# Performance work log

Measured on AMD Instinct MI355X. Metric: run time of the kernel, lower is better.

## Reference

```python
import jax, jax.numpy as jnp
import numpy as np

N_NODES = 50000
N_EDGES = 800000
IN_DIM = 128
HID = 64
N_GRAPHS = 256


def gcn_conv(x, W, b, src, dst, num_nodes):
    """PyG GCNConv: add self-loops, sym norm D^-1/2 (A+I) D^-1/2, linear, bias."""
    h = x @ W  # [N, out]
    loop = jnp.arange(num_nodes)
    s = jnp.concatenate([src, loop])
    d = jnp.concatenate([dst, loop])
    ones = jnp.ones(d.shape, h.dtype)
    deg = jax.ops.segment_sum(ones, d, num_segments=num_nodes)
    dinv = jnp.where(deg > 0, jax.lax.rsqrt(deg), 0.0)
    norm = dinv[s] * dinv[d]  # [E+N]
    msg = h[s] * norm[:, None]  # gather + scale (memory bound)
    out = jax.ops.segment_sum(msg, d, num_segments=num_nodes)  # scatter-add
    return out + b


def setup_inputs() -> dict:
    key = jax.random.key(0)
    ks = jax.random.split(key, 8)
    x = jax.random.normal(ks[0], (N_NODES, IN_DIM), dtype=jnp.float32)
    edge_index = jax.random.randint(ks[1], (2, N_EDGES), 0, N_NODES, dtype=jnp.int64)
    batch = jnp.sort(jax.random.randint(ks[2], (N_NODES,), 0, N_GRAPHS, dtype=jnp.int64))
    W1 = jax.random.normal(ks[3], (IN_DIM, HID), dtype=jnp.float32) / np.sqrt(IN_DIM)
    b1 = jnp.zeros((HID,), jnp.float32)
    W2 = jax.random.normal(ks[4], (HID, HID), dtype=jnp.float32) / np.sqrt(HID)
    b2 = jnp.zeros((HID,), jnp.float32)
    Wl = jax.random.normal(ks[5], (HID, 1), dtype=jnp.float32) / np.sqrt(HID)
    bl = jnp.zeros((1,), jnp.float32)
    return {"x": x, "W1": W1, "b1": b1, "W2": W2, "b2": b2,
            "Wl": Wl, "bl": bl, "edge_index": edge_index, "batch": batch}


def reference(x, W1, b1, W2, b2, Wl, bl, edge_index, batch):
    n = x.shape[0]
    src, dst = edge_index[0], edge_index[1]
    h = jax.nn.relu(gcn_conv(x, W1, b1, src, dst, n))
    # dropout is identity in eval mode
    h = jax.nn.relu(gcn_conv(h, W2, b2, src, dst, n))
    ones = jnp.ones((n,), h.dtype)
    counts = jax.ops.segment_sum(ones, batch, num_segments=N_GRAPHS)
    pooled = jax.ops.segment_sum(h, batch, num_segments=N_GRAPHS)
    pooled = pooled / jnp.maximum(counts, 1.0)[:, None]  # global_mean_pool
    return (pooled @ Wl + bl).reshape(-1)  # [N_GRAPHS]
```

## Files before the change

kernel.cpp:

```cpp
#include <hip/hip_runtime.h>
#include <math.h>

__global__ void zero32(int* __restrict__ p, int n) {
    int i = blockIdx.x * blockDim.x + threadIdx.x;
    if (i < n) p[i] = 0;
}

__global__ void hist_dst(const int* __restrict__ dst, int* __restrict__ cnt, int E) {
    int e = blockIdx.x * blockDim.x + threadIdx.x;
    if (e < E) atomicAdd(&cnt[dst[e]], 1);
}

__global__ __launch_bounds__(256) void scan1_dinv(const int* __restrict__ cnt,
                                                  int* __restrict__ excl,
                                                  int* __restrict__ sums,
                                                  float* __restrict__ dinv, int n) {
    int i = blockIdx.x * 256 + threadIdx.x;
    int v = (i < n) ? cnt[i] : 0;
    if (i < n) dinv[i] = rsqrtf((float)(v + 1));
    int lane = threadIdx.x & 63;
    int w = threadIdx.x >> 6;
    int s = v;
#pragma unroll
    for (int off = 1; off < 64; off <<= 1) {
        int t = __shfl_up(s, off, 64);
        if (lane >= off) s += t;
    }
    __shared__ int wsum[4];
    if (lane == 63) wsum[w] = s;
    __syncthreads();
    int woff = 0;
#pragma unroll
    for (int k = 0; k < 3; ++k) if (k < w) woff += wsum[k];
    int incl = s + woff;
    if (i < n) excl[i] = incl - v;
    if (threadIdx.x == 255) sums[blockIdx.x] = incl;
}

__global__ __launch_bounds__(256) void scan2(int* __restrict__ sums, int nb) {
    int t = threadIdx.x;
    int v = (t < nb) ? sums[t] : 0;
    int lane = t & 63;
    int w = t >> 6;
    int s = v;
#pragma unroll
    for (int off = 1; off < 64; off <<= 1) {
        int u = __shfl_up(s, off, 64);
        if (lane >= off) s += u;
    }
    __shared__ int wsum[4];
    if (lane == 63) wsum[w] = s;
    __syncthreads();
    int woff = 0;
#pragma unroll
    for (int k = 0; k < 3; ++k) if (k < w) woff += wsum[k];
    int incl = s + woff;
    if (t < nb) sums[t] = incl - v;
}

__global__ __launch_bounds__(256) void scan3(const int* __restrict__ excl,
                                             const int* __restrict__ sums,
                                             int* __restrict__ rowptr,
                                             int* __restrict__ cursor, int n, int E) {
    int i = blockIdx.x * 256 + threadIdx.x;
    if (i < n) {
        int r = excl[i] + sums[i >> 8];
        rowptr[i] = r;
        cursor[i] = r;
    }
    if (i == n) rowptr[n] = E;
}

__global__ void fill_col16(const int* __restrict__ src, const int* __restrict__ dst,
                           int* __restrict__ cursor, unsigned short* __restrict__ col,
                           int E, int n) {
    const int g    = blockIdx.x & 7;
    const int nblk = gridDim.x >> 3;
    const int bid  = blockIdx.x >> 3;
    const int lo = (int)(((long)g * n) >> 3);
    const int hi = (int)(((long)(g + 1) * n) >> 3);
    for (long e = (long)bid * blockDim.x + threadIdx.x; e < E;
         e += (long)nblk * blockDim.x) {
        int d = dst[e];
        if (d < lo || d >= hi) continue;
        int p = atomicAdd(&cursor[d], 1);
        col[p] = (unsigned short)src[e];
    }
}

#define RL(x, k) __int_as_float(__builtin_amdgcn_readlane(__float_as_int(x), (k)))

template <int K>
__global__ __launch_bounds__(256) void gemm_bcast_scaled(const float* __restrict__ X,
                                                         const float* __restrict__ W,
                                                         const float* __restrict__ dinv,
                                                         float* __restrict__ Y, int n) {
    const int lane = threadIdx.x & 63;
    const long wid = (((long)blockIdx.x * blockDim.x) + threadIdx.x) >> 6;
    const long nw  = ((long)gridDim.x * blockDim.x) >> 6;

    float wr[K];
#pragma unroll
    for (int k = 0; k < K; ++k) wr[k] = W[k * 64 + lane];
#pragma unroll
    for (int k = 0; k < K; ++k) asm volatile("" : "+v"(wr[k]));

    long r = wid;
    if (r >= n) return;
    float xa = X[r * K + lane];
    float xb = 0.f;
    if constexpr (K > 64) xb = X[r * K + 64 + lane];
    float dv = dinv[r];

    while (true) {
        long rn = r + nw;
        bool more = rn < n;
        long rc = more ? rn : r;
        float xan = X[rc * K + lane];
        float xbn = 0.f;
        if constexpr (K > 64) xbn = X[rc * K + 64 + lane];
        float dvn = dinv[rc];

        float a0 = 0.f, a1 = 0.f, a2 = 0.f, a3 = 0.f;
#pragma unroll
        for (int k = 0; k < 64; k += 4) {
            a0 = fmaf(RL(xa, k + 0), wr[k + 0], a0);
            a1 = fmaf(RL(xa, k + 1), wr[k + 1], a1);
            a2 = fmaf(RL(xa, k + 2), wr[k + 2], a2);
            a3 = fmaf(RL(xa, k + 3), wr[k + 3], a3);
        }
        if constexpr (K > 64) {
#pragma unroll
            for (int k = 0; k < 64; k += 4) {
                a0 = fmaf(RL(xb, k + 0), wr[64 + k + 0], a0);
                a1 = fmaf(RL(xb, k + 1), wr[64 + k + 1], a1);
                a2 = fmaf(RL(xb, k + 2), wr[64 + k + 2], a2);
                a3 = fmaf(RL(xb, k + 3), wr[64 + k + 3], a3);
            }
        }
        Y[r * 64 + lane] = dv * ((a0 + a1) + (a2 + a3));
        if (!more) break;
        r = rn;
        xa = xan;
        xb = xbn;
        dv = dvn;
    }
}

__device__ __forceinline__ void agg2(const float* __restrict__ Hp,
                                     const int* __restrict__ rowptr,
                                     const unsigned short* __restrict__ col,
                                     long vA, long vB, int j, bool hasB,
                                     float& sumA, float& sumB) {
    float a0 = Hp[vA * 64 + j], a1 = 0.f, a2 = 0.f, a3 = 0.f;
    float b0 = 0.f, b1 = 0.f, b2 = 0.f, b3 = 0.f;
    int pA = rowptr[vA], pA1 = rowptr[vA + 1];
    int pB = 0, pB1 = 0;
    if (hasB) { b0 = Hp[vB * 64 + j]; pB = rowptr[vB]; pB1 = rowptr[vB + 1]; }
    if ((pA & 1) && pA < pA1) { a1 += Hp[(long)col[pA] * 64 + j]; ++pA; }
    if ((pB & 1) && pB < pB1) { b1 += Hp[(long)col[pB] * 64 + j]; ++pB; }
    unsigned int cA01 = *(const unsigned int*)(col + pA);
    unsigned int cA23 = *(const unsigned int*)(col + pA + 2);
    unsigned int cB01 = *(const unsigned int*)(col + pB);
    unsigned int cB23 = *(const unsigned int*)(col + pB + 2);
    while (pA + 4 <= pA1 && pB + 4 <= pB1) {
        unsigned int nA01 = *(const unsigned int*)(col + pA + 4);
        unsigned int nA23 = *(const unsigned int*)(col + pA + 6);
        unsigned int nB01 = *(const unsigned int*)(col + pB + 4);
        unsigned int nB23 = *(const unsigned int*)(col + pB + 6);
        float hA0 = Hp[(long)(cA01 & 0xFFFFu) * 64 + j];
        float hA1 = Hp[(long)(cA01 >> 16) * 64 + j];
        float hA2 = Hp[(long)(cA23 & 0xFFFFu) * 64 + j];
        float hA3 = Hp[(long)(cA23 >> 16) * 64 + j];
        float hB0 = Hp[(long)(cB01 & 0xFFFFu) * 64 + j];
        float hB1 = Hp[(long)(cB01 >> 16) * 64 + j];
        float hB2 = Hp[(long)(cB23 & 0xFFFFu) * 64 + j];
        float hB3 = Hp[(long)(cB23 >> 16) * 64 + j];
        a0 += hA0; a1 += hA1; a2 += hA2; a3 += hA3;
        b0 += hB0; b1 += hB1; b2 += hB2; b3 += hB3;
        cA01 = nA01; cA23 = nA23; cB01 = nB01; cB23 = nB23;
        pA += 4; pB += 4;
    }
    for (; pA + 4 <= pA1; pA += 4) {
        float h0 = Hp[(long)(cA01 & 0xFFFFu) * 64 + j];
        float h1 = Hp[(long)(cA01 >> 16) * 64 + j];
        float h2 = Hp[(long)(cA23 & 0xFFFFu) * 64 + j];
        float h3 = Hp[(long)(cA23 >> 16) * 64 + j];
        a0 += h0; a1 += h1; a2 += h2; a3 += h3;
        cA01 = *(const unsigned int*)(col + pA + 4);
        cA23 = *(const unsigned int*)(col + pA + 6);
    }
    for (; pA < pA1; ++pA) a1 += Hp[(long)col[pA] * 64 + j];
    for (; pB + 4 <= pB1; pB += 4) {
        float h0 = Hp[(long)(cB01 & 0xFFFFu) * 64 + j];
        float h1 = Hp[(long)(cB01 >> 16) * 64 + j];
        float h2 = Hp[(long)(cB23 & 0xFFFFu) * 64 + j];
        float h3 = Hp[(long)(cB23 >> 16) * 64 + j];
        b0 += h0; b1 += h1; b2 += h2; b3 += h3;
        cB01 = *(const unsigned int*)(col + pB + 4);
        cB23 = *(const unsigned int*)(col + pB + 6);
    }
    for (; pB < pB1; ++pB) b1 += Hp[(long)col[pB] * 64 + j];
    sumA = (a0 + a1) + (a2 + a3);
    sumB = (b0 + b1) + (b2 + b3);
}

__global__ __launch_bounds__(256) void agg_gemm64(const float* __restrict__ Hp,
                                                  const int* __restrict__ rowptr,
                                                  const unsigned short* __restrict__ col,
                                                  const float* __restrict__ dinv,
                                                  const float* __restrict__ bias,
                                                  const float* __restrict__ W2,
                                                  float* __restrict__ out, int n) {
    const int j = threadIdx.x & 63;
    const long wid = (((long)blockIdx.x * blockDim.x) + threadIdx.x) >> 6;
    const long NW  = ((long)gridDim.x * blockDim.x) >> 6;
    float wr[64];
#pragma unroll
    for (int k = 0; k < 64; ++k) wr[k] = W2[k * 64 + j];
#pragma unroll
    for (int k = 0; k < 64; ++k) asm volatile("" : "+v"(wr[k]));
    const float bj = bias[j];
    for (long vA = wid; vA < n; vA += 2 * NW) {
        long vB = vA + NW;
        bool hasB = vB < n;
        float sA, sB;
        agg2(Hp, rowptr, col, vA, vB, j, hasB, sA, sB);
        float diA = dinv[vA];
        float diB = hasB ? dinv[vB] : 0.f;
        float gA = fmaxf(diA * sA + bj, 0.f);
        float gB = fmaxf(diB * sB + bj, 0.f);
        float a0 = 0.f, a1 = 0.f, a2 = 0.f, a3 = 0.f;
        float b0 = 0.f, b1 = 0.f, b2 = 0.f, b3 = 0.f;
#pragma unroll
        for (int k = 0; k < 64; k += 4) {
            float w0 = wr[k + 0], w1 = wr[k + 1], w2 = wr[k + 2], w3 = wr[k + 3];
            a0 = fmaf(RL(gA, k + 0), w0, a0);
            b0 = fmaf(RL(gB, k + 0), w0, b0);
            a1 = fmaf(RL(gA, k + 1), w1, a1);
            b1 = fmaf(RL(gB, k + 1), w1, b1);
            a2 = fmaf(RL(gA, k + 2), w2, a2);
            b2 = fmaf(RL(gB, k + 2), w2, b2);
            a3 = fmaf(RL(gA, k + 3), w3, a3);
            b3 = fmaf(RL(gB, k + 3), w3, b3);
        }
        out[vA * 64 + j] = diA * ((a0 + a1) + (a2 + a3));
        if (hasB) out[vB * 64 + j] = diB * ((b0 + b1) + (b2 + b3));
    }
}

__global__ __launch_bounds__(256) void agg_pool(const float* __restrict__ Hp,
                                                const int* __restrict__ rowptr,
                                                const unsigned short* __restrict__ col,
                                                const float* __restrict__ dinv,
                                                const float* __restrict__ bias,
                                                const float* __restrict__ Wl,
                                                const int* __restrict__ batch,
                                                float* __restrict__ part,
                                                float* __restrict__ partc, int n) {
    __shared__ float lp[256];
    __shared__ float lc[256];
    lp[threadIdx.x] = 0.f;
    lc[threadIdx.x] = 0.f;
    __syncthreads();
    const int j  = threadIdx.x & 63;
    const int wv = threadIdx.x >> 6;
    const float bj  = bias[j];
    const float wlj = Wl[j];
    const long wid = (long)blockIdx.x * 4 + wv;
    const long NW  = (long)gridDim.x * 4;
    for (long vA = wid; vA < n; vA += 2 * NW) {
        long vB = vA + NW;
        bool hasB = vB < n;
        float sA, sB;
        agg2(Hp, rowptr, col, vA, vB, j, hasB, sA, sB);
        float diA = dinv[vA];
        float diB = hasB ? dinv[vB] : 0.f;
        float valA = fmaxf(diA * sA + bj, 0.f) * wlj;
        float valB = fmaxf(diB * sB + bj, 0.f) * wlj;
#pragma unroll
        for (int off = 32; off > 0; off >>= 1) {
            valA += __shfl_down(valA, off, 64);
            valB += __shfl_down(valB, off, 64);
        }
        if (j == 0) {
            atomicAdd(&lp[batch[vA]], valA);
            atomicAdd(&lc[batch[vA]], 1.0f);
            if (hasB) {
                atomicAdd(&lp[batch[vB]], valB);
                atomicAdd(&lc[batch[vB]], 1.0f);
            }
        }
    }
    __syncthreads();
    long o = (long)blockIdx.x * 256 + threadIdx.x;
    part[o]  = lp[threadIdx.x];
    partc[o] = lc[threadIdx.x];
}

__global__ __launch_bounds__(256) void pool_final(const float* __restrict__ part,
                                                  const float* __restrict__ partc,
                                                  const float* __restrict__ bl,
                                                  float* __restrict__ out, int nblk) {
    int g = blockIdx.x;
    int t = threadIdx.x;
    float s = 0.f, c = 0.f;
    for (int b = t; b < nblk; b += 256) {
        s += part[(long)b * 256 + g];
        c += partc[(long)b * 256 + g];
    }
    __shared__ float sp[256];
    __shared__ float sc[256];
    sp[t] = s;
    sc[t] = c;
    __syncthreads();
    for (int off = 128; off > 0; off >>= 1) {
        if (t < off) { sp[t] += sp[t + off]; sc[t] += sc[t + off]; }
        __syncthreads();
    }
    if (t == 0) out[g] = sp[0] / fmaxf(sc[0], 1.0f) + bl[0];
}

extern "C" void kernel_launch(void* const* d_in, const int* in_sizes, int n_in,
                              void* d_out, int out_size, void* d_ws, size_t ws_size,
                              hipStream_t stream) {
    const float* x  = (const float*)d_in[0];
    const float* W1 = (const float*)d_in[1];
    const float* b1 = (const float*)d_in[2];
    const float* W2 = (const float*)d_in[3];
    const float* b2 = (const float*)d_in[4];
    const float* Wl = (const float*)d_in[5];
    const float* bl = (const float*)d_in[6];
    const int* edge_index = (const int*)d_in[7];
    const int* batch      = (const int*)d_in[8];

    const int n = in_sizes[0] / 128;
    const int E = in_sizes[7] / 2;
    const int G = out_size;
    const int* src = edge_index;
    const int* dst = edge_index + E;

    char* ws = (char*)d_ws;
    size_t off = 0;
    auto alloc = [&](size_t bytes) { void* p = ws + off; off = (off + bytes + 255) & ~(size_t)255; return p; };
    int*            cntv   = (int*)           alloc((size_t)n * 4);
    float*          dinv   = (float*)         alloc((size_t)n * 4);
    int*            rowptr = (int*)           alloc((size_t)(n + 1) * 4);
    int*            cursor = (int*)           alloc((size_t)n * 4);
    int*            excl   = (int*)           alloc((size_t)n * 4);
    int*            sums   = (int*)           alloc((size_t)256 * 4);
    unsigned short* col    = (unsigned short*)alloc((size_t)E * 2 + 64);
    float*          bufA   = (float*)         alloc((size_t)n * 64 * 4);
    float*          bufB   = (float*)         alloc((size_t)n * 64 * 4);
    const int PBLK = 2048;
    float*          part   = (float*)         alloc((size_t)PBLK * 256 * 4);
    float*          partc  = (float*)         alloc((size_t)PBLK * 256 * 4);

    const int T = 256;
    const int nchunks = (n + 255) / 256;
    zero32<<<(n + T - 1) / T, T, 0, stream>>>(cntv, n);
    hist_dst<<<(E + T - 1) / T, T, 0, stream>>>(dst, cntv, E);
    scan1_dinv<<<nchunks, T, 0, stream>>>(cntv, excl, sums, dinv, n);
    scan2<<<1, T, 0, stream>>>(sums, nchunks);
    scan3<<<(n + 1 + T - 1) / T, T, 0, stream>>>(excl, sums, rowptr, cursor, n, E);
    fill_col16<<<1024, T, 0, stream>>>(src, dst, cursor, col, E, n);

    gemm_bcast_scaled<128><<<768, T, 0, stream>>>(x, W1, dinv, bufA, n);
    agg_gemm64<<<2048, T, 0, stream>>>(bufA, rowptr, col, dinv, b1, W2, bufB, n);
    agg_pool<<<PBLK, T, 0, stream>>>(bufB, rowptr, col, dinv, b2, Wl, batch, part, partc, n);
    pool_final<<<G, T, 0, stream>>>(part, partc, bl, (float*)d_out, PBLK);
}
```

Before: 203.4 us.

## Record edge rank in histogram pass and add 2-deep prefetch in GEMM

```diff
diff --git a/kernel.cpp b/kernel.cpp
--- a/kernel.cpp
+++ b/kernel.cpp
@@ -6,9 +6,10 @@
     if (i < n) p[i] = 0;
 }
 
-__global__ void hist_dst(const int* __restrict__ dst, int* __restrict__ cnt, int E) {
+__global__ void hist_rank(const int* __restrict__ dst, int* __restrict__ cnt,
+                          unsigned short* __restrict__ rank, int E) {
     int e = blockIdx.x * blockDim.x + threadIdx.x;
-    if (e < E) atomicAdd(&cnt[dst[e]], 1);
+    if (e < E) rank[e] = (unsigned short)atomicAdd(&cnt[dst[e]], 1);
 }
 
 __global__ __launch_bounds__(256) void scan1_dinv(const int* __restrict__ cnt,
@@ -60,20 +61,16 @@
 
 __global__ __launch_bounds__(256) void scan3(const int* __restrict__ excl,
                                              const int* __restrict__ sums,
-                                             int* __restrict__ rowptr,
-                                             int* __restrict__ cursor, int n, int E) {
+                                             int* __restrict__ rowptr, int n, int E) {
     int i = blockIdx.x * 256 + threadIdx.x;
-    if (i < n) {
-        int r = excl[i] + sums[i >> 8];
-        rowptr[i] = r;
-        cursor[i] = r;
-    }
+    if (i < n) rowptr[i] = excl[i] + sums[i >> 8];
     if (i == n) rowptr[n] = E;
 }
 
-__global__ void fill_col16(const int* __restrict__ src, const int* __restrict__ dst,
-                           int* __restrict__ cursor, unsigned short* __restrict__ col,
-                           int E, int n) {
+__global__ void fill_place(const int* __restrict__ src, const int* __restrict__ dst,
+                           const unsigned short* __restrict__ rank,
+                           const int* __restrict__ rowptr,
+                           unsigned short* __restrict__ col, int E, int n) {
     const int g    = blockIdx.x & 7;
     const int nblk = gridDim.x >> 3;
     const int bid  = blockIdx.x >> 3;
@@ -83,8 +80,7 @@
          e += (long)nblk * blockDim.x) {
         int d = dst[e];
         if (d < lo || d >= hi) continue;
-        int p = atomicAdd(&cursor[d], 1);
-        col[p] = (unsigned short)src[e];
+        col[rowptr[d] + rank[e]] = (unsigned short)src[e];
     }
 }
 
@@ -105,45 +101,51 @@
 #pragma unroll
     for (int k = 0; k < K; ++k) asm volatile("" : "+v"(wr[k]));
 
-    long r = wid;
-    if (r >= n) return;
-    float xa = X[r * K + lane];
-    float xb = 0.f;
-    if constexpr (K > 64) xb = X[r * K + 64 + lane];
-    float dv = dinv[r];
+    long r0 = wid;
+    if (r0 >= n) return;
+    float xa0 = X[r0 * K + lane];
+    float xb0 = 0.f;
+    if constexpr (K > 64) xb0 = X[r0 * K + 64 + lane];
+    float dv0 = dinv[r0];
+
+    long r1 = r0 + nw;
+    bool h1 = r1 < n;
+    long rc1 = h1 ? r1 : r0;
+    float xa1 = X[rc1 * K + lane];
+    float xb1 = 0.f;
+    if constexpr (K > 64) xb1 = X[rc1 * K + 64 + lane];
+    float dv1 = dinv[rc1];
 
     while (true) {
-        long rn = r + nw;
-        bool more = rn < n;
-        long rc = more ? rn : r;
-        float xan = X[rc * K + lane];
-        float xbn = 0.f;
-        if constexpr (K > 64) xbn = X[rc * K + 64 + lane];
-        float dvn = dinv[rc];
+        long r2 = r1 + nw;
+        bool h2 = h1 && (r2 < n);
+        long rc2 = h2 ? r2 : r0;
+        float xa2 = X[rc2 * K + lane];
+        float xb2 = 0.f;
+        if constexpr (K > 64) xb2 = X[rc2 * K + 64 + lane];
+        float dv2 = dinv[rc2];
 
         float a0 = 0.f, a1 = 0.f, a2 = 0.f, a3 = 0.f;
 #pragma unroll
         for (int k = 0; k < 64; k += 4) {
-            a0 = fmaf(RL(xa, k + 0), wr[k + 0], a0);
-            a1 = fmaf(RL(xa, k + 1), wr[k + 1], a1);
-            a2 = fmaf(RL(xa, k + 2), wr[k + 2], a2);
-            a3 = fmaf(RL(xa, k + 3), wr[k + 3], a3);
+            a0 = fmaf(RL(xa0, k + 0), wr[k + 0], a0);
+            a1 = fmaf(RL(xa0, k + 1), wr[k + 1], a1);
+            a2 = fmaf(RL(xa0, k + 2), wr[k + 2], a2);
+            a3 = fmaf(RL(xa0, k + 3), wr[k + 3], a3);
         }
         if constexpr (K > 64) {
 #pragma unroll
             for (int k = 0; k < 64; k += 4) {
-                a0 = fmaf(RL(xb, k + 0), wr[64 + k + 0], a0);
-                a1 = fmaf(RL(xb, k + 1), wr[64 + k + 1], a1);
-                a2 = fmaf(RL(xb, k + 2), wr[64 + k + 2], a2);
-                a3 = fmaf(RL(xb, k + 3), wr[64 + k + 3], a3);
+                a0 = fmaf(RL(xb0, k + 0), wr[64 + k + 0], a0);
+                a1 = fmaf(RL(xb0, k + 1), wr[64 + k + 1], a1);
+                a2 = fmaf(RL(xb0, k + 2), wr[64 + k + 2], a2);
+                a3 = fmaf(RL(xb0, k + 3), wr[64 + k + 3], a3);
             }
         }
-        Y[r * 64 + lane] = dv * ((a0 + a1) + (a2 + a3));
-        if (!more) break;
-        r = rn;
-        xa = xan;
-        xb = xbn;
-        dv = dvn;
+        Y[r0 * 64 + lane] = dv0 * ((a0 + a1) + (a2 + a3));
+        if (!h1) break;
+        r0 = r1; xa0 = xa1; xb0 = xb1; dv0 = dv1;
+        r1 = r2; h1 = h2; xa1 = xa2; xb1 = xb2; dv1 = dv2;
     }
 }
 
@@ -346,9 +348,9 @@
     int*            cntv   = (int*)           alloc((size_t)n * 4);
     float*          dinv   = (float*)         alloc((size_t)n * 4);
     int*            rowptr = (int*)           alloc((size_t)(n + 1) * 4);
-    int*            cursor = (int*)           alloc((size_t)n * 4);
     int*            excl   = (int*)           alloc((size_t)n * 4);
     int*            sums   = (int*)           alloc((size_t)256 * 4);
+    unsigned short* rank   = (unsigned short*)alloc((size_t)E * 2);
     unsigned short* col    = (unsigned short*)alloc((size_t)E * 2 + 64);
     float*          bufA   = (float*)         alloc((size_t)n * 64 * 4);
     float*          bufB   = (float*)         alloc((size_t)n * 64 * 4);
@@ -359,11 +361,11 @@
     const int T = 256;
     const int nchunks = (n + 255) / 256;
     zero32<<<(n + T - 1) / T, T, 0, stream>>>(cntv, n);
-    hist_dst<<<(E + T - 1) / T, T, 0, stream>>>(dst, cntv, E);
+    hist_rank<<<(E + T - 1) / T, T, 0, stream>>>(dst, cntv, rank, E);
     scan1_dinv<<<nchunks, T, 0, stream>>>(cntv, excl, sums, dinv, n);
     scan2<<<1, T, 0, stream>>>(sums, nchunks);
-    scan3<<<(n + 1 + T - 1) / T, T, 0, stream>>>(excl, sums, rowptr, cursor, n, E);
-    fill_col16<<<1024, T, 0, stream>>>(src, dst, cursor, col, E, n);
+    scan3<<<(n + 1 + T - 1) / T, T, 0, stream>>>(excl, sums, rowptr, n, E);
+    fill_place<<<1024, T, 0, stream>>>(src, dst, rank, rowptr, col, E, n);
 
     gemm_bcast_scaled<128><<<768, T, 0, stream>>>(x, W1, dinv, bufA, n);
     agg_gemm64<<<2048, T, 0, stream>>>(bufA, rowptr, col, dinv, b1, W2, bufB, n);
```

Result: faster. 186.4 us (-8.4%).
